# Performance work log

Hardware: AMD Instinct MI355X
Metric: run time of the kernel (lower is better)

## Reference

```python
import jax, jax.numpy as jnp
import numpy as np

B, N_VIS, N_TXT = 2, 2048, 256
N_HEAD, HEAD_DIM = 16, 64
C = N_HEAD * HEAD_DIM  # 1024
EPS = 1e-6


def setup_inputs() -> dict:
    key = jax.random.key(0)
    ks = jax.random.split(key, 24)
    s = 0.02
    inp = {
        'vis_x': jax.random.normal(ks[0], (B, N_VIS, C), jnp.float32),
        'txt_x': jax.random.normal(ks[1], (B, N_TXT, C), jnp.float32),
        'rope_cos': jax.random.uniform(ks[2], (N_VIS, HEAD_DIM), jnp.float32, -1.0, 1.0),
        'rope_sin': jax.random.uniform(ks[3], (N_VIS, HEAD_DIM), jnp.float32, -1.0, 1.0),
    }
    names = ['vis_qw', 'vis_kw', 'vis_vw', 'vis_ow', 'txt_qw', 'txt_kw', 'txt_vw', 'txt_ow']
    for i, n in enumerate(names):
        inp[n] = jax.random.normal(ks[4 + i], (C, C), jnp.float32) * s
        inp[n[:-1] + 'b'] = jnp.zeros((C,), jnp.float32)
    for n in ['vis_qn', 'vis_kn', 'txt_qn', 'txt_kn']:
        inp[n] = jnp.ones((HEAD_DIM,), jnp.float32)
    return inp


def _heads(x, w, b):
    # x: [B,N,C] -> [B,H,N,D]  (torch Linear: x @ W.T + b)
    y = x @ w.T + b
    Bn, N, _ = y.shape
    return y.reshape(Bn, N, N_HEAD, HEAD_DIM).transpose(0, 2, 1, 3)


def _rmsnorm(x, g):
    return x * jax.lax.rsqrt(jnp.mean(x * x, axis=-1, keepdims=True) + EPS) * g


def _rope(x, cos, sin):
    # interleaved-pair rotation: pairs (x0,x1) -> (-x1, x0)
    xr, xi = x[..., 0::2], x[..., 1::2]
    rot = jnp.stack([-xi, xr], axis=-1).reshape(x.shape)
    return x * cos[None, None] + rot * sin[None, None]


def reference(vis_x, txt_x, rope_cos, rope_sin,
              vis_qw, vis_qb, vis_kw, vis_kb, vis_vw, vis_vb, vis_ow, vis_ob,
              txt_qw, txt_qb, txt_kw, txt_kb, txt_vw, txt_vb, txt_ow, txt_ob,
              vis_qn, vis_kn, txt_qn, txt_kn):
    q_vis = _rmsnorm(_heads(vis_x, vis_qw, vis_qb), vis_qn)
    k_vis = _rmsnorm(_heads(vis_x, vis_kw, vis_kb), vis_kn)
    v_vis = _heads(vis_x, vis_vw, vis_vb)
    q_txt = _rmsnorm(_heads(txt_x, txt_qw, txt_qb), txt_qn)
    k_txt = _rmsnorm(_heads(txt_x, txt_kw, txt_kb), txt_kn)
    v_txt = _heads(txt_x, txt_vw, txt_vb)

    q_vis = _rope(q_vis, rope_cos, rope_sin)
    k_vis = _rope(k_vis, rope_cos, rope_sin)

    q = jnp.concatenate([q_txt, q_vis], axis=2)  # [B,H,S,D]
    k = jnp.concatenate([k_txt, k_vis], axis=2)
    v = jnp.concatenate([v_txt, v_vis], axis=2)

    scale = 1.0 / jnp.sqrt(jnp.asarray(HEAD_DIM, q.dtype))
    scores = jnp.einsum('bhqd,bhkd->bhqk', q, k) * scale
    attn = jax.nn.softmax(scores, axis=-1)
    out = jnp.einsum('bhqk,bhkd->bhqd', attn, v)  # [B,H,S,D]

    txt_out = out[:, :, :N_TXT, :].transpose(0, 2, 1, 3).reshape(q.shape[0], N_TXT, C)
    vis_out = out[:, :, N_TXT:, :].transpose(0, 2, 1, 3).reshape(q.shape[0], N_VIS, C)
    vis_out = vis_out @ vis_ow.T + vis_ob
    txt_out = txt_out @ txt_ow.T + txt_ob
    return (vis_out, txt_out)
```

## Files before the change

### kernel.cpp

```cpp
#include <hip/hip_runtime.h>

typedef _Float16 h8 __attribute__((ext_vector_type(8)));
typedef _Float16 h4 __attribute__((ext_vector_type(4)));
typedef _Float16 h2 __attribute__((ext_vector_type(2)));
typedef float f4 __attribute__((ext_vector_type(4)));
typedef float f16x16 __attribute__((ext_vector_type(16)));

#define LOG2E 1.44269504088896340736f

__device__ __forceinline__ void gload_lds16(const void* g, void* l) {
    __builtin_amdgcn_global_load_lds(
        (const __attribute__((address_space(1))) void*)g,
        (__attribute__((address_space(3))) void*)l, 16, 0, 0);
}

struct CastArgs { const float* src[10]; _Float16* dst[10]; };

__global__ __launch_bounds__(256) void cast_all_kernel(CastArgs a) {
    int blk = blockIdx.x;
    int seg, rel;
    if (blk < 4096)      { seg = 0; rel = blk; }
    else if (blk < 4608) { seg = 1; rel = blk - 4096; }
    else { int t = blk - 4608; seg = 2 + (t >> 10); rel = t & 1023; }
    long base = ((long)rel * 256 + threadIdx.x) * 4;
    float4 v = *(const float4*)(a.src[seg] + base);
    h4 o = { (_Float16)v.x, (_Float16)v.y, (_Float16)v.z, (_Float16)v.w };
    *(h4*)(a.dst[seg] + base) = o;
}

struct GemmDesc {
    const _Float16* A[2];
    const _Float16* W[2];
    char*           C[2];
    const float*    bias[2][3];
    long bsA[2];
    long aoff[2];
    long bsC[2];
    int  mshift[2];
    int  mcut;
};

template<bool OUT_F32>
__global__ __launch_bounds__(256)
void gemm_kernel(GemmDesc g, int K, int N)
{
    __shared__ __align__(16) _Float16 As[128 * 64];
    __shared__ __align__(16) _Float16 Bs[128 * 64];
    const int lane = threadIdx.x & 63;
    const int wave = threadIdx.x >> 6;
    const int mtile = blockIdx.y, ntile = blockIdx.x;

    const int seg = mtile >= g.mcut;
    const int mloc = mtile - (seg ? g.mcut : 0);
    const int bidx = mloc >> g.mshift[seg];
    const int min_ = mloc & ((1 << g.mshift[seg]) - 1);
    const _Float16* Ab = g.A[seg] + (long)bidx * g.bsA[seg] + g.aoff[seg]
                         + (long)min_ * 128 * K;
    const _Float16* Bb = g.W[seg] + (long)ntile * 128 * K;
    const long crow0 = (long)bidx * g.bsC[seg] + (long)min_ * 128 * N;

    const int wr = wave >> 1, wc = wave & 1;
    f4 acc[4][4] = {};

    for (int kt = 0; kt < K; kt += 64) {
        __syncthreads();
#pragma unroll
        for (int it = 0; it < 4; ++it) {
            int r = wave * 32 + it * 8 + (lane >> 3);
            int lc = (lane & 7) ^ (r & 7);
            gload_lds16((const char*)(Ab + (long)r * K + kt) + lc * 16,
                        (char*)As + (wave * 32 + it * 8) * 128);
            gload_lds16((const char*)(Bb + (long)r * K + kt) + lc * 16,
                        (char*)Bs + (wave * 32 + it * 8) * 128);
        }
        asm volatile("s_waitcnt vmcnt(0)" ::: "memory");
        __syncthreads();
#pragma unroll
        for (int kk = 0; kk < 2; ++kk) {
            h8 af[4], bf[4];
#pragma unroll
            for (int m = 0; m < 4; ++m) {
                int row = wr * 64 + m * 16 + (lane & 15);
                int pc = (kk * 4 + (lane >> 4)) ^ (row & 7);
                af[m] = *(const h8*)(&As[row * 64 + pc * 8]);
            }
#pragma unroll
            for (int n = 0; n < 4; ++n) {
                int row = wc * 64 + n * 16 + (lane & 15);
                int pc = (kk * 4 + (lane >> 4)) ^ (row & 7);
                bf[n] = *(const h8*)(&Bs[row * 64 + pc * 8]);
            }
#pragma unroll
            for (int m = 0; m < 4; ++m)
#pragma unroll
                for (int n = 0; n < 4; ++n)
                    acc[m][n] = __builtin_amdgcn_mfma_f32_16x16x32_f16(
                        af[m], bf[n], acc[m][n], 0, 0, 0);
        }
    }

#pragma unroll
    for (int n = 0; n < 4; ++n) {
        int col = ntile * 128 + wc * 64 + n * 16 + (lane & 15);
        const float* bp = (col < 1024) ? g.bias[seg][0]
                        : (col < 2048) ? g.bias[seg][1] : g.bias[seg][2];
        float bv = bp[col & 1023];
#pragma unroll
        for (int m = 0; m < 4; ++m) {
            int lrow = wr * 64 + m * 16 + ((lane >> 4) << 2);
#pragma unroll
            for (int r = 0; r < 4; ++r) {
                float v = acc[m][n][r] + bv;
                long off = crow0 + (long)(lrow + r) * N + col;
                if (OUT_F32) ((float*)g.C[seg])[off] = v;
                else         ((_Float16*)g.C[seg])[off] = (_Float16)v;
            }
        }
    }
}

__global__ __launch_bounds__(256)
void pass2_kernel(const _Float16* __restrict__ Yv, const _Float16* __restrict__ Yt,
                  const float* __restrict__ gqv, const float* __restrict__ gkv_,
                  const float* __restrict__ gqt, const float* __restrict__ gkt,
                  const float* __restrict__ rc, const float* __restrict__ rs,
                  _Float16* __restrict__ Q, _Float16* __restrict__ Kd,
                  _Float16* __restrict__ Vt)
{
    const int blk = blockIdx.x;
    const int is_vis = blk < 4096;
    const _Float16* Y; const float *gq, *gk; int m, nlog2;
    if (is_vis) { Y = Yv; gq = gqv; gk = gkv_; m = blk; nlog2 = 11; }
    else        { Y = Yt; gq = gqt; gk = gkt; m = blk - 4096; nlog2 = 8; }
    const int lane = threadIdx.x & 63;
    const int wave = threadIdx.x >> 6;
    const int b = m >> nlog2;
    const int n = m - (b << nlog2);
    const int npos = is_vis ? (256 + n) : n;
    const _Float16* y = Y + (long)m * 3072;
    const int d = lane;
    float cosv = 0.f, sinv = 0.f;
    if (is_vis) { cosv = rc[n * 64 + d]; sinv = rs[n * 64 + d]; }
    const float gqs = gq[d] * (0.125f * LOG2E);
    const float gks = gk[d];

#pragma unroll
    for (int hh = 0; hh < 4; ++hh) {
        int h = wave * 4 + hh;
        long ob = (((long)b * 16 + h) * 2304 + npos) * 64 + d;
        float q = (float)y[h * 64 + d];
        float ss = q * q;
#pragma unroll
        for (int o = 1; o < 64; o <<= 1) ss += __shfl_xor(ss, o);
        float qv = q * rsqrtf(ss * (1.0f / 64.0f) + 1e-6f) * gqs;
        if (is_vis) {
            float p = __shfl_xor(qv, 1);
            qv = qv * cosv + ((d & 1) ? p : -p) * sinv;
        }
        Q[ob] = (_Float16)qv;
        float k = (float)y[1024 + h * 64 + d];
        ss = k * k;
#pragma unroll
        for (int o = 1; o < 64; o <<= 1) ss += __shfl_xor(ss, o);
        float kv = k * rsqrtf(ss * (1.0f / 64.0f) + 1e-6f) * gks;
        if (is_vis) {
            float p = __shfl_xor(kv, 1);
            kv = kv * cosv + ((d & 1) ? p : -p) * sinv;
        }
        Kd[ob] = (_Float16)kv;
        float v = (float)y[2048 + h * 64 + d];
        Vt[(((long)b * 16 + h) * 64 + d) * 2304 + npos] = (_Float16)v;
    }
}

__device__ __forceinline__ void attn_stage(const char* Kt, const char* Vt, char* S,
                                           int bufB, int t,
                                           int gK0, int gK1, int gV0, int gV1,
                                           int ldsW) {
    const char* kt = Kt + (long)t * 8192;
    const char* vt = Vt + (long)t * 128;
    gload_lds16(kt + gK0, S + bufB + ldsW);
    gload_lds16(kt + gK1, S + bufB + 4096 + ldsW);
    gload_lds16(vt + gV0, S + 16384 + bufB + ldsW);
    gload_lds16(vt + gV1, S + 16384 + bufB + 4096 + ldsW);
}

__device__ __forceinline__ void attn_tile(const char* S, int bufB, const int* off,
                                          const h8* qf, f16x16* oacc, float& psum) {
    const f16x16 kZero = {};
    const h2 one2 = {(_Float16)1.f, (_Float16)1.f};
#pragma unroll
    for (int kblk = 0; kblk < 2; ++kblk) {
        f16x16 st;
        {
            h8 ka = *(const h8*)(S + bufB + kblk * 4096 + off[0]);
            st = __builtin_amdgcn_mfma_f32_32x32x16_f16(ka, qf[0], kZero, 0, 0, 0);
        }
#pragma unroll
        for (int ds = 1; ds < 4; ++ds) {
            h8 ka = *(const h8*)(S + bufB + kblk * 4096 + off[ds]);
            st = __builtin_amdgcn_mfma_f32_32x32x16_f16(ka, qf[ds], st, 0, 0, 0);
        }
        float p[16];
#pragma unroll
        for (int r = 0; r < 16; ++r) p[r] = exp2f(st[r]);
#pragma unroll
        for (int kb = 0; kb < 2; ++kb) {
            unsigned w0 = __builtin_bit_cast(unsigned,
                __builtin_amdgcn_cvt_pkrtz(p[8 * kb + 0], p[8 * kb + 1]));
            unsigned w1 = __builtin_bit_cast(unsigned,
                __builtin_amdgcn_cvt_pkrtz(p[8 * kb + 2], p[8 * kb + 3]));
            unsigned w2 = __builtin_bit_cast(unsigned,
                __builtin_amdgcn_cvt_pkrtz(p[8 * kb + 4], p[8 * kb + 5]));
            unsigned w3 = __builtin_bit_cast(unsigned,
                __builtin_amdgcn_cvt_pkrtz(p[8 * kb + 6], p[8 * kb + 7]));
            psum = __builtin_amdgcn_fdot2(__builtin_bit_cast(h2, w0), one2, psum, false);
            psum = __builtin_amdgcn_fdot2(__builtin_bit_cast(h2, w1), one2, psum, false);
            psum = __builtin_amdgcn_fdot2(__builtin_bit_cast(h2, w2), one2, psum, false);
            psum = __builtin_amdgcn_fdot2(__builtin_bit_cast(h2, w3), one2, psum, false);
            asm("v_permlane32_swap_b32 %0, %1" : "+v"(w0), "+v"(w2));
            asm("v_permlane32_swap_b32 %0, %1" : "+v"(w1), "+v"(w3));
            union { unsigned u[4]; h8 v; } pa;
            pa.u[0] = w0; pa.u[1] = w1; pa.u[2] = w2; pa.u[3] = w3;
#pragma unroll
            for (int dblk = 0; dblk < 2; ++dblk) {
                h8 vb = *(const h8*)(S + 16384 + bufB + dblk * 4096 + off[kblk * 2 + kb]);
                oacc[dblk] = __builtin_amdgcn_mfma_f32_32x32x16_f16(
                    pa.v, vb, oacc[dblk], 0, 0, 0);
            }
        }
    }
}

__global__ __launch_bounds__(256)
void attn_kernel(const _Float16* __restrict__ Qg,
                 const _Float16* __restrict__ Kg,
                 const _Float16* __restrict__ Vg,
                 _Float16* __restrict__ Op,
                 float* __restrict__ Lp)
{
    __shared__ __align__(16) char S[32768];
    const int lane = threadIdx.x & 63;
    const int wave = threadIdx.x >> 6;
    const int l31 = lane & 31, hi = lane >> 5;
    const int d0 = blockIdx.x;
    const int id = (d0 & 7) * 144 + (d0 >> 3);
    const int split = id / 576;
    const int rem = id - split * 576;
    const int bh = rem / 18;
    const int qb = rem - bh * 18;
    const int b = bh >> 4, h = bh & 15;
    const _Float16* Qbh = Qg + (long)bh * 2304 * 64;
    const char* Kt = (const char*)(Kg + (long)bh * 2304 * 64) + (long)split * 1152 * 128;
    const char* Vt = (const char*)(Vg + (long)bh * 64 * 2304) + (long)split * 1152 * 2;
    _Float16* Ops = Op + (long)split * 4718592;
    float* Lps = Lp + (long)split * 73728;
    const int q0 = qb * 128 + wave * 32;

    h8 qf[4];
#pragma unroll
    for (int ds = 0; ds < 4; ++ds)
        qf[ds] = *(const h8*)(Qbh + (long)(q0 + l31) * 64 + ds * 16 + hi * 8);

    const int sg16 = ((lane & 7) ^ (lane >> 3)) * 16;
    const int rK = wave * 8 + (lane >> 3);
    const int gK0 = rK * 128 + sg16;
    const int gK1 = gK0 + 32 * 128;
    const int gV0 = rK * 4608 + sg16;
    const int gV1 = gV0 + 32 * 4608;
    const int ldsW = wave * 1024;
    int off[4];
#pragma unroll
    for (int j = 0; j < 4; ++j)
        off[j] = l31 * 128 + (((j * 2 + hi) ^ (l31 & 7)) * 16);

    f16x16 oacc[2] = {};
    float psum = 0.f;

    attn_stage(Kt, Vt, S, 0, 0, gK0, gK1, gV0, gV1, ldsW);
    asm volatile("s_waitcnt vmcnt(0)" ::: "memory");
    __syncthreads();

#pragma unroll 1
    for (int pr = 0; pr < 9; ++pr) {
        const int t = pr * 2;
        attn_stage(Kt, Vt, S, 8192, t + 1, gK0, gK1, gV0, gV1, ldsW);
        __builtin_amdgcn_s_setprio(1);
        attn_tile(S, 0, off, qf, oacc, psum);
        __builtin_amdgcn_s_setprio(0);
        asm volatile("s_waitcnt vmcnt(0)" ::: "memory");
        __syncthreads();
        if (pr != 8)
            attn_stage(Kt, Vt, S, 0, t + 2, gK0, gK1, gV0, gV1, ldsW);
        __builtin_amdgcn_s_setprio(1);
        attn_tile(S, 8192, off, qf, oacc, psum);
        __builtin_amdgcn_s_setprio(0);
        asm volatile("s_waitcnt vmcnt(0)" ::: "memory");
        __syncthreads();
    }

    float lsum = psum + __shfl_xor(psum, 32);
    if (hi == 0) Lps[(long)bh * 2304 + q0 + l31] = lsum;
#pragma unroll
    for (int dblk = 0; dblk < 2; ++dblk) {
        int dcol = h * 64 + dblk * 32 + l31;
#pragma unroll
        for (int r = 0; r < 16; ++r) {
            int qrow = q0 + (r & 3) + 8 * (r >> 2) + 4 * hi;
            Ops[((long)b * 2304 + qrow) * 1024 + dcol] = (_Float16)oacc[dblk][r];
        }
    }
}

__global__ __launch_bounds__(256)
void combine_kernel(const _Float16* __restrict__ Op,
                    const float* __restrict__ Lp,
                    _Float16* __restrict__ Oh)
{
    long i = ((long)blockIdx.x * 256 + threadIdx.x) * 8;
    h8 a = *(const h8*)(Op + i);
    h8 c = *(const h8*)(Op + 4718592 + i);
    long row = i >> 10;
    int bb = row >= 2304;
    int n = (int)row - bb * 2304;
    int h = ((int)i & 1023) >> 6;
    long lidx = ((long)(bb * 16 + h)) * 2304 + n;
    float inv = 1.0f / (Lp[lidx] + Lp[73728 + lidx]);
    h8 o;
#pragma unroll
    for (int j = 0; j < 8; ++j)
        o[j] = (_Float16)(((float)a[j] + (float)c[j]) * inv);
    *(h8*)(Oh + i) = o;
}

extern "C" void kernel_launch(void* const* d_in, const int* in_sizes, int n_in,
                              void* d_out, int out_size, void* d_ws, size_t ws_size,
                              hipStream_t stream)
{
    const float* vis_x    = (const float*)d_in[0];
    const float* txt_x    = (const float*)d_in[1];
    const float* rope_cos = (const float*)d_in[2];
    const float* rope_sin = (const float*)d_in[3];
    const float* vis_qw = (const float*)d_in[4];
    const float* vis_qb = (const float*)d_in[5];
    const float* vis_kw = (const float*)d_in[6];
    const float* vis_kb = (const float*)d_in[7];
    const float* vis_vw = (const float*)d_in[8];
    const float* vis_vb = (const float*)d_in[9];
    const float* vis_ow = (const float*)d_in[10];
    const float* vis_ob = (const float*)d_in[11];
    const float* txt_qw = (const float*)d_in[12];
    const float* txt_qb = (const float*)d_in[13];
    const float* txt_kw = (const float*)d_in[14];
    const float* txt_kb = (const float*)d_in[15];
    const float* txt_vw = (const float*)d_in[16];
    const float* txt_vb = (const float*)d_in[17];
    const float* txt_ow = (const float*)d_in[18];
    const float* txt_ob = (const float*)d_in[19];
    const float* vis_qn = (const float*)d_in[20];
    const float* vis_kn = (const float*)d_in[21];
    const float* txt_qn = (const float*)d_in[22];
    const float* txt_kn = (const float*)d_in[23];

    char* ws = (char*)d_ws;
    _Float16* Xvis  = (_Float16*)(ws);
    _Float16* Xtxt  = (_Float16*)(ws + 8388608);
    _Float16* Qh    = (_Float16*)(ws);
    _Float16* WqkvV = (_Float16*)(ws + 9437184);
    _Float16* WqkvT = (_Float16*)(ws + 15728640);
    _Float16* WoV   = (_Float16*)(ws + 22020096);
    _Float16* WoT   = (_Float16*)(ws + 24117248);
    _Float16* Yvis  = (_Float16*)(ws + 26214400);
    _Float16* Ytxt  = (_Float16*)(ws + 51380224);
    _Float16* OpP   = (_Float16*)(ws + 26214400);
    float*    LpP   = (float*)   (ws + 45088768);
    _Float16* Oh    = (_Float16*)(ws + 26214400);
    _Float16* Kh    = (_Float16*)(ws + 54525952);
    _Float16* Vth   = (_Float16*)(ws + 63963136);

    CastArgs ca;
    ca.src[0] = vis_x;  ca.dst[0] = Xvis;
    ca.src[1] = txt_x;  ca.dst[1] = Xtxt;
    ca.src[2] = vis_qw; ca.dst[2] = WqkvV;
    ca.src[3] = vis_kw; ca.dst[3] = WqkvV + 1048576;
    ca.src[4] = vis_vw; ca.dst[4] = WqkvV + 2097152;
    ca.src[5] = txt_qw; ca.dst[5] = WqkvT;
    ca.src[6] = txt_kw; ca.dst[6] = WqkvT + 1048576;
    ca.src[7] = txt_vw; ca.dst[7] = WqkvT + 2097152;
    ca.src[8] = vis_ow; ca.dst[8] = WoV;
    ca.src[9] = txt_ow; ca.dst[9] = WoT;
    cast_all_kernel<<<12800, 256, 0, stream>>>(ca);

    GemmDesc gq;
    gq.A[0] = Xvis;  gq.A[1] = Xtxt;
    gq.W[0] = WqkvV; gq.W[1] = WqkvT;
    gq.C[0] = (char*)Yvis; gq.C[1] = (char*)Ytxt;
    gq.bias[0][0] = vis_qb; gq.bias[0][1] = vis_kb; gq.bias[0][2] = vis_vb;
    gq.bias[1][0] = txt_qb; gq.bias[1][1] = txt_kb; gq.bias[1][2] = txt_vb;
    gq.bsA[0] = 0; gq.bsA[1] = 0;
    gq.aoff[0] = 0; gq.aoff[1] = 0;
    gq.bsC[0] = 0; gq.bsC[1] = 0;
    gq.mshift[0] = 5; gq.mshift[1] = 5;
    gq.mcut = 32;
    gemm_kernel<false><<<dim3(24, 36), 256, 0, stream>>>(gq, 1024, 3072);

    pass2_kernel<<<4608, 256, 0, stream>>>(
        Yvis, Ytxt, vis_qn, vis_kn, txt_qn, txt_kn, rope_cos, rope_sin,
        Qh, Kh, Vth);

    attn_kernel<<<1152, 256, 0, stream>>>(Qh, Kh, Vth, OpP, LpP);
    combine_kernel<<<2304, 256, 0, stream>>>(OpP, LpP, Oh);

    GemmDesc go;
    go.A[0] = Oh; go.A[1] = Oh;
    go.W[0] = WoV; go.W[1] = WoT;
    go.C[0] = (char*)d_out; go.C[1] = (char*)((float*)d_out + 4194304);
    go.bias[0][0] = vis_ob; go.bias[0][1] = vis_ob; go.bias[0][2] = vis_ob;
    go.bias[1][0] = txt_ob; go.bias[1][1] = txt_ob; go.bias[1][2] = txt_ob;
    go.bsA[0] = 2359296;  go.bsA[1] = 2359296;
    go.aoff[0] = 262144;  go.aoff[1] = 0;
    go.bsC[0] = 2097152;  go.bsC[1] = 262144;
    go.mshift[0] = 4; go.mshift[1] = 1;
    go.mcut = 32;
    gemm_kernel<true><<<dim3(8, 36), 256, 0, stream>>>(go, 1024, 1024);
}
```

Baseline: 199.6 us.

## Remap GEMM tiles per XCD, vectorize norm/rope pass, widen attention split-K

The GEMM grid becomes 1D and is remapped so each XCD works on a contiguous block of M/N tiles, aiming at better L2 reuse. The norm/RoPE pass now handles one row per wave with 8-wide vector loads and stores instead of per-element shuffles. Attention can split the KV range four ways instead of two when the workspace is large enough, issues the two score MFMA chains interleaved, and sets a launch-bounds occupancy hint. The combine kernel is generalized to sum a variable number of splits, at the cost of extra partial-output traffic.

```diff
diff --git a/kernel.cpp b/kernel.cpp
--- a/kernel.cpp
+++ b/kernel.cpp
@@ -42,13 +42,17 @@
 
 template<bool OUT_F32>
 __global__ __launch_bounds__(256)
-void gemm_kernel(GemmDesc g, int K, int N)
+void gemm_kernel(GemmDesc g, int K, int N, int gm, int gn, int xgn)
 {
     __shared__ __align__(16) _Float16 As[128 * 64];
     __shared__ __align__(16) _Float16 Bs[128 * 64];
     const int lane = threadIdx.x & 63;
     const int wave = threadIdx.x >> 6;
-    const int mtile = blockIdx.y, ntile = blockIdx.x;
+    const int lid = blockIdx.x;
+    const int xcd = lid & 7;
+    const int r0 = lid >> 3;
+    const int mtile = (xcd / xgn) * gm + (r0 % gm);
+    const int ntile = (xcd % xgn) * gn + (r0 / gm);
 
     const int seg = mtile >= g.mcut;
     const int mloc = mtile - (seg ? g.mcut : 0);
@@ -119,6 +123,36 @@
     }
 }
 
+__device__ __forceinline__ float ssum8(h8 v) {
+    float s = 0.f;
+#pragma unroll
+    for (int j = 0; j < 8; ++j) { float f = (float)v[j]; s += f * f; }
+    return s;
+}
+__device__ __forceinline__ float red8(float s) {
+    s += __shfl_xor(s, 1); s += __shfl_xor(s, 2); s += __shfl_xor(s, 4);
+    return s;
+}
+__device__ __forceinline__ h8 norm_rope(h8 v, float rs_, const float* g, float gmul,
+                                        const float* cs, const float* sn, int vis) {
+    float f[8];
+#pragma unroll
+    for (int j = 0; j < 8; ++j) f[j] = (float)v[j] * rs_ * g[j] * gmul;
+    h8 o;
+    if (vis) {
+#pragma unroll
+        for (int j = 0; j < 8; j += 2) {
+            float a = f[j], b = f[j + 1];
+            o[j]     = (_Float16)(a * cs[j]     - b * sn[j]);
+            o[j + 1] = (_Float16)(b * cs[j + 1] + a * sn[j + 1]);
+        }
+    } else {
+#pragma unroll
+        for (int j = 0; j < 8; ++j) o[j] = (_Float16)f[j];
+    }
+    return o;
+}
+
 __global__ __launch_bounds__(256)
 void pass2_kernel(const _Float16* __restrict__ Yv, const _Float16* __restrict__ Yt,
                   const float* __restrict__ gqv, const float* __restrict__ gkv_,
@@ -127,49 +161,63 @@
                   _Float16* __restrict__ Q, _Float16* __restrict__ Kd,
                   _Float16* __restrict__ Vt)
 {
-    const int blk = blockIdx.x;
-    const int is_vis = blk < 4096;
-    const _Float16* Y; const float *gq, *gk; int m, nlog2;
-    if (is_vis) { Y = Yv; gq = gqv; gk = gkv_; m = blk; nlog2 = 11; }
-    else        { Y = Yt; gq = gqt; gk = gkt; m = blk - 4096; nlog2 = 8; }
+    const int wave = threadIdx.x >> 6;
     const int lane = threadIdx.x & 63;
-    const int wave = threadIdx.x >> 6;
-    const int b = m >> nlog2;
-    const int n = m - (b << nlog2);
-    const int npos = is_vis ? (256 + n) : n;
-    const _Float16* y = Y + (long)m * 3072;
-    const int d = lane;
-    float cosv = 0.f, sinv = 0.f;
-    if (is_vis) { cosv = rc[n * 64 + d]; sinv = rs[n * 64 + d]; }
-    const float gqs = gq[d] * (0.125f * LOG2E);
-    const float gks = gk[d];
-
-#pragma unroll
-    for (int hh = 0; hh < 4; ++hh) {
-        int h = wave * 4 + hh;
-        long ob = (((long)b * 16 + h) * 2304 + npos) * 64 + d;
-        float q = (float)y[h * 64 + d];
-        float ss = q * q;
-#pragma unroll
-        for (int o = 1; o < 64; o <<= 1) ss += __shfl_xor(ss, o);
-        float qv = q * rsqrtf(ss * (1.0f / 64.0f) + 1e-6f) * gqs;
-        if (is_vis) {
-            float p = __shfl_xor(qv, 1);
-            qv = qv * cosv + ((d & 1) ? p : -p) * sinv;
-        }
-        Q[ob] = (_Float16)qv;
-        float k = (float)y[1024 + h * 64 + d];
-        ss = k * k;
-#pragma unroll
-        for (int o = 1; o < 64; o <<= 1) ss += __shfl_xor(ss, o);
-        float kv = k * rsqrtf(ss * (1.0f / 64.0f) + 1e-6f) * gks;
-        if (is_vis) {
-            float p = __shfl_xor(kv, 1);
-            kv = kv * cosv + ((d & 1) ? p : -p) * sinv;
-        }
-        Kd[ob] = (_Float16)kv;
-        float v = (float)y[2048 + h * 64 + d];
-        Vt[(((long)b * 16 + h) * 64 + d) * 2304 + npos] = (_Float16)v;
+    const int row = blockIdx.x * 4 + wave;
+    const int is_vis = row < 4096;
+    const _Float16* y;
+    const float *gq, *gk;
+    int b, n, npos;
+    if (is_vis) {
+        y = Yv + (long)row * 3072; gq = gqv; gk = gkv_;
+        b = row >> 11; n = row & 2047; npos = 256 + n;
+    } else {
+        int r2 = row - 4096;
+        y = Yt + (long)r2 * 3072; gq = gqt; gk = gkt;
+        b = r2 >> 8; n = r2 & 255; npos = n;
+    }
+    const int h0 = lane >> 3;
+    const int d0 = (lane & 7) * 8;
+
+    h8 q0 = *(const h8*)(y + lane * 8);
+    h8 q1 = *(const h8*)(y + 512 + lane * 8);
+    h8 k0 = *(const h8*)(y + 1024 + lane * 8);
+    h8 k1 = *(const h8*)(y + 1536 + lane * 8);
+    h8 v0 = *(const h8*)(y + 2048 + lane * 8);
+    h8 v1 = *(const h8*)(y + 2560 + lane * 8);
+
+    float ga[8], gb[8];
+    *(float4*)(ga)     = *(const float4*)(gq + d0);
+    *(float4*)(ga + 4) = *(const float4*)(gq + d0 + 4);
+    *(float4*)(gb)     = *(const float4*)(gk + d0);
+    *(float4*)(gb + 4) = *(const float4*)(gk + d0 + 4);
+    float cs[8], sn[8];
+    if (is_vis) {
+        *(float4*)(cs)     = *(const float4*)(rc + n * 64 + d0);
+        *(float4*)(cs + 4) = *(const float4*)(rc + n * 64 + d0 + 4);
+        *(float4*)(sn)     = *(const float4*)(rs + n * 64 + d0);
+        *(float4*)(sn + 4) = *(const float4*)(rs + n * 64 + d0 + 4);
+    }
+
+    const float rq0 = rsqrtf(red8(ssum8(q0)) * (1.0f / 64.0f) + 1e-6f);
+    const float rq1 = rsqrtf(red8(ssum8(q1)) * (1.0f / 64.0f) + 1e-6f);
+    const float rk0 = rsqrtf(red8(ssum8(k0)) * (1.0f / 64.0f) + 1e-6f);
+    const float rk1 = rsqrtf(red8(ssum8(k1)) * (1.0f / 64.0f) + 1e-6f);
+
+    const float qmul = 0.125f * LOG2E;
+    const long obA = (((long)b * 16 + h0)      * 2304 + npos) * 64 + d0;
+    const long obB = (((long)b * 16 + h0 + 8)  * 2304 + npos) * 64 + d0;
+    *(h8*)(Q + obA)  = norm_rope(q0, rq0, ga, qmul, cs, sn, is_vis);
+    *(h8*)(Q + obB)  = norm_rope(q1, rq1, ga, qmul, cs, sn, is_vis);
+    *(h8*)(Kd + obA) = norm_rope(k0, rk0, gb, 1.0f, cs, sn, is_vis);
+    *(h8*)(Kd + obB) = norm_rope(k1, rk1, gb, 1.0f, cs, sn, is_vis);
+
+    const long vbA = ((long)(b * 16 + h0)     * 64 + d0) * 2304 + npos;
+    const long vbB = ((long)(b * 16 + h0 + 8) * 64 + d0) * 2304 + npos;
+#pragma unroll
+    for (int j = 0; j < 8; ++j) {
+        Vt[vbA + (long)j * 2304] = v0[j];
+        Vt[vbB + (long)j * 2304] = v1[j];
     }
 }
 
@@ -185,74 +233,83 @@
     gload_lds16(vt + gV1, S + 16384 + bufB + 4096 + ldsW);
 }
 
+__device__ __forceinline__ void pv_half(const float* p, const char* S, int vbase,
+                                        const int* off, int kblk,
+                                        f16x16* oacc, float& psum) {
+    const h2 one2 = {(_Float16)1.f, (_Float16)1.f};
+#pragma unroll
+    for (int kb = 0; kb < 2; ++kb) {
+        unsigned w0 = __builtin_bit_cast(unsigned,
+            __builtin_amdgcn_cvt_pkrtz(p[8 * kb + 0], p[8 * kb + 1]));
+        unsigned w1 = __builtin_bit_cast(unsigned,
+            __builtin_amdgcn_cvt_pkrtz(p[8 * kb + 2], p[8 * kb + 3]));
+        unsigned w2 = __builtin_bit_cast(unsigned,
+            __builtin_amdgcn_cvt_pkrtz(p[8 * kb + 4], p[8 * kb + 5]));
+        unsigned w3 = __builtin_bit_cast(unsigned,
+            __builtin_amdgcn_cvt_pkrtz(p[8 * kb + 6], p[8 * kb + 7]));
+        psum = __builtin_amdgcn_fdot2(__builtin_bit_cast(h2, w0), one2, psum, false);
+        psum = __builtin_amdgcn_fdot2(__builtin_bit_cast(h2, w1), one2, psum, false);
+        psum = __builtin_amdgcn_fdot2(__builtin_bit_cast(h2, w2), one2, psum, false);
+        psum = __builtin_amdgcn_fdot2(__builtin_bit_cast(h2, w3), one2, psum, false);
+        asm("v_permlane32_swap_b32 %0, %1" : "+v"(w0), "+v"(w2));
+        asm("v_permlane32_swap_b32 %0, %1" : "+v"(w1), "+v"(w3));
+        union { unsigned u[4]; h8 v; } pa;
+        pa.u[0] = w0; pa.u[1] = w1; pa.u[2] = w2; pa.u[3] = w3;
+#pragma unroll
+        for (int dblk = 0; dblk < 2; ++dblk) {
+            h8 vb = *(const h8*)(S + vbase + dblk * 4096 + off[kblk * 2 + kb]);
+            oacc[dblk] = __builtin_amdgcn_mfma_f32_32x32x16_f16(
+                pa.v, vb, oacc[dblk], 0, 0, 0);
+        }
+    }
+}
+
 __device__ __forceinline__ void attn_tile(const char* S, int bufB, const int* off,
                                           const h8* qf, f16x16* oacc, float& psum) {
     const f16x16 kZero = {};
-    const h2 one2 = {(_Float16)1.f, (_Float16)1.f};
-#pragma unroll
-    for (int kblk = 0; kblk < 2; ++kblk) {
-        f16x16 st;
-        {
-            h8 ka = *(const h8*)(S + bufB + kblk * 4096 + off[0]);
-            st = __builtin_amdgcn_mfma_f32_32x32x16_f16(ka, qf[0], kZero, 0, 0, 0);
-        }
-#pragma unroll
-        for (int ds = 1; ds < 4; ++ds) {
-            h8 ka = *(const h8*)(S + bufB + kblk * 4096 + off[ds]);
-            st = __builtin_amdgcn_mfma_f32_32x32x16_f16(ka, qf[ds], st, 0, 0, 0);
-        }
-        float p[16];
-#pragma unroll
-        for (int r = 0; r < 16; ++r) p[r] = exp2f(st[r]);
-#pragma unroll
-        for (int kb = 0; kb < 2; ++kb) {
-            unsigned w0 = __builtin_bit_cast(unsigned,
-                __builtin_amdgcn_cvt_pkrtz(p[8 * kb + 0], p[8 * kb + 1]));
-            unsigned w1 = __builtin_bit_cast(unsigned,
-                __builtin_amdgcn_cvt_pkrtz(p[8 * kb + 2], p[8 * kb + 3]));
-            unsigned w2 = __builtin_bit_cast(unsigned,
-                __builtin_amdgcn_cvt_pkrtz(p[8 * kb + 4], p[8 * kb + 5]));
-            unsigned w3 = __builtin_bit_cast(unsigned,
-                __builtin_amdgcn_cvt_pkrtz(p[8 * kb + 6], p[8 * kb + 7]));
-            psum = __builtin_amdgcn_fdot2(__builtin_bit_cast(h2, w0), one2, psum, false);
-            psum = __builtin_amdgcn_fdot2(__builtin_bit_cast(h2, w1), one2, psum, false);
-            psum = __builtin_amdgcn_fdot2(__builtin_bit_cast(h2, w2), one2, psum, false);
-            psum = __builtin_amdgcn_fdot2(__builtin_bit_cast(h2, w3), one2, psum, false);
-            asm("v_permlane32_swap_b32 %0, %1" : "+v"(w0), "+v"(w2));
-            asm("v_permlane32_swap_b32 %0, %1" : "+v"(w1), "+v"(w3));
-            union { unsigned u[4]; h8 v; } pa;
-            pa.u[0] = w0; pa.u[1] = w1; pa.u[2] = w2; pa.u[3] = w3;
-#pragma unroll
-            for (int dblk = 0; dblk < 2; ++dblk) {
-                h8 vb = *(const h8*)(S + 16384 + bufB + dblk * 4096 + off[kblk * 2 + kb]);
-                oacc[dblk] = __builtin_amdgcn_mfma_f32_32x32x16_f16(
-                    pa.v, vb, oacc[dblk], 0, 0, 0);
-            }
-        }
-    }
-}
-
-__global__ __launch_bounds__(256)
+    f16x16 st0, st1;
+    {
+        h8 ka0 = *(const h8*)(S + bufB + off[0]);
+        h8 ka1 = *(const h8*)(S + bufB + 4096 + off[0]);
+        st0 = __builtin_amdgcn_mfma_f32_32x32x16_f16(ka0, qf[0], kZero, 0, 0, 0);
+        st1 = __builtin_amdgcn_mfma_f32_32x32x16_f16(ka1, qf[0], kZero, 0, 0, 0);
+    }
+#pragma unroll
+    for (int ds = 1; ds < 4; ++ds) {
+        h8 ka0 = *(const h8*)(S + bufB + off[ds]);
+        h8 ka1 = *(const h8*)(S + bufB + 4096 + off[ds]);
+        st0 = __builtin_amdgcn_mfma_f32_32x32x16_f16(ka0, qf[ds], st0, 0, 0, 0);
+        st1 = __builtin_amdgcn_mfma_f32_32x32x16_f16(ka1, qf[ds], st1, 0, 0, 0);
+    }
+    float p0[16], p1[16];
+#pragma unroll
+    for (int r = 0; r < 16; ++r) { p0[r] = exp2f(st0[r]); p1[r] = exp2f(st1[r]); }
+    pv_half(p0, S, 16384 + bufB, off, 0, oacc, psum);
+    pv_half(p1, S, 16384 + bufB, off, 1, oacc, psum);
+}
+
+__global__ __launch_bounds__(256, 4)
 void attn_kernel(const _Float16* __restrict__ Qg,
                  const _Float16* __restrict__ Kg,
                  const _Float16* __restrict__ Vg,
                  _Float16* __restrict__ Op,
-                 float* __restrict__ Lp)
+                 float* __restrict__ Lp,
+                 int nt, int cpx)
 {
     __shared__ __align__(16) char S[32768];
     const int lane = threadIdx.x & 63;
     const int wave = threadIdx.x >> 6;
     const int l31 = lane & 31, hi = lane >> 5;
     const int d0 = blockIdx.x;
-    const int id = (d0 & 7) * 144 + (d0 >> 3);
+    const int id = (d0 & 7) * cpx + (d0 >> 3);
     const int split = id / 576;
     const int rem = id - split * 576;
     const int bh = rem / 18;
     const int qb = rem - bh * 18;
     const int b = bh >> 4, h = bh & 15;
     const _Float16* Qbh = Qg + (long)bh * 2304 * 64;
-    const char* Kt = (const char*)(Kg + (long)bh * 2304 * 64) + (long)split * 1152 * 128;
-    const char* Vt = (const char*)(Vg + (long)bh * 64 * 2304) + (long)split * 1152 * 2;
+    const char* Kt = (const char*)(Kg + (long)bh * 2304 * 64) + (long)split * nt * 8192;
+    const char* Vt = (const char*)(Vg + (long)bh * 64 * 2304) + (long)split * nt * 128;
     _Float16* Ops = Op + (long)split * 4718592;
     float* Lps = Lp + (long)split * 73728;
     const int q0 = qb * 128 + wave * 32;
@@ -281,22 +338,37 @@
     asm volatile("s_waitcnt vmcnt(0)" ::: "memory");
     __syncthreads();
 
+    int t = 0;
 #pragma unroll 1
-    for (int pr = 0; pr < 9; ++pr) {
-        const int t = pr * 2;
+    for (int pr = 0; pr < (nt - 1) >> 1; ++pr) {
         attn_stage(Kt, Vt, S, 8192, t + 1, gK0, gK1, gV0, gV1, ldsW);
         __builtin_amdgcn_s_setprio(1);
         attn_tile(S, 0, off, qf, oacc, psum);
         __builtin_amdgcn_s_setprio(0);
         asm volatile("s_waitcnt vmcnt(0)" ::: "memory");
         __syncthreads();
-        if (pr != 8)
-            attn_stage(Kt, Vt, S, 0, t + 2, gK0, gK1, gV0, gV1, ldsW);
+        attn_stage(Kt, Vt, S, 0, t + 2, gK0, gK1, gV0, gV1, ldsW);
         __builtin_amdgcn_s_setprio(1);
         attn_tile(S, 8192, off, qf, oacc, psum);
         __builtin_amdgcn_s_setprio(0);
         asm volatile("s_waitcnt vmcnt(0)" ::: "memory");
         __syncthreads();
+        t += 2;
+    }
+    if (nt & 1) {
+        __builtin_amdgcn_s_setprio(1);
+        attn_tile(S, 0, off, qf, oacc, psum);
+        __builtin_amdgcn_s_setprio(0);
+    } else {
+        attn_stage(Kt, Vt, S, 8192, nt - 1, gK0, gK1, gV0, gV1, ldsW);
+        __builtin_amdgcn_s_setprio(1);
+        attn_tile(S, 0, off, qf, oacc, psum);
+        __builtin_amdgcn_s_setprio(0);
+        asm volatile("s_waitcnt vmcnt(0)" ::: "memory");
+        __syncthreads();
+        __builtin_amdgcn_s_setprio(1);
+        attn_tile(S, 8192, off, qf, oacc, psum);
+        __builtin_amdgcn_s_setprio(0);
     }
 
     float lsum = psum + __shfl_xor(psum, 32);
@@ -315,21 +387,26 @@
 __global__ __launch_bounds__(256)
 void combine_kernel(const _Float16* __restrict__ Op,
                     const float* __restrict__ Lp,
-                    _Float16* __restrict__ Oh)
+                    _Float16* __restrict__ Oh, int ns)
 {
     long i = ((long)blockIdx.x * 256 + threadIdx.x) * 8;
-    h8 a = *(const h8*)(Op + i);
-    h8 c = *(const h8*)(Op + 4718592 + i);
     long row = i >> 10;
     int bb = row >= 2304;
     int n = (int)row - bb * 2304;
     int h = ((int)i & 1023) >> 6;
     long lidx = ((long)(bb * 16 + h)) * 2304 + n;
-    float inv = 1.0f / (Lp[lidx] + Lp[73728 + lidx]);
+    float l = 0.f;
+    float acc[8] = {};
+    for (int s = 0; s < ns; ++s) {
+        l += Lp[(long)s * 73728 + lidx];
+        h8 a = *(const h8*)(Op + (long)s * 4718592 + i);
+#pragma unroll
+        for (int j = 0; j < 8; ++j) acc[j] += (float)a[j];
+    }
+    float inv = 1.0f / l;
     h8 o;
 #pragma unroll
-    for (int j = 0; j < 8; ++j)
-        o[j] = (_Float16)(((float)a[j] + (float)c[j]) * inv);
+    for (int j = 0; j < 8; ++j) o[j] = (_Float16)(acc[j] * inv);
     *(h8*)(Oh + i) = o;
 }
 
@@ -372,11 +449,16 @@
     _Float16* WoT   = (_Float16*)(ws + 24117248);
     _Float16* Yvis  = (_Float16*)(ws + 26214400);
     _Float16* Ytxt  = (_Float16*)(ws + 51380224);
-    _Float16* OpP   = (_Float16*)(ws + 26214400);
-    float*    LpP   = (float*)   (ws + 45088768);
-    _Float16* Oh    = (_Float16*)(ws + 26214400);
     _Float16* Kh    = (_Float16*)(ws + 54525952);
     _Float16* Vth   = (_Float16*)(ws + 63963136);
+
+    const int ns = (ws_size >= 112328704) ? 4 : 2;
+    const int nt = (ns == 4) ? 9 : 18;
+    _Float16* OpP;
+    if (ns == 4) OpP = (_Float16*)(ws + 73400320);
+    else         OpP = (_Float16*)(ws + 26214400);
+    float* LpP = (float*)((char*)OpP + (size_t)ns * 9437184);
+    _Float16* Oh = OpP;
 
     CastArgs ca;
     ca.src[0] = vis_x;  ca.dst[0] = Xvis;
@@ -402,14 +484,14 @@
     gq.bsC[0] = 0; gq.bsC[1] = 0;
     gq.mshift[0] = 5; gq.mshift[1] = 5;
     gq.mcut = 32;
-    gemm_kernel<false><<<dim3(24, 36), 256, 0, stream>>>(gq, 1024, 3072);
-
-    pass2_kernel<<<4608, 256, 0, stream>>>(
+    gemm_kernel<false><<<864, 256, 0, stream>>>(gq, 1024, 3072, 9, 12, 2);
+
+    pass2_kernel<<<1152, 256, 0, stream>>>(
         Yvis, Ytxt, vis_qn, vis_kn, txt_qn, txt_kn, rope_cos, rope_sin,
         Qh, Kh, Vth);
 
-    attn_kernel<<<1152, 256, 0, stream>>>(Qh, Kh, Vth, OpP, LpP);
-    combine_kernel<<<2304, 256, 0, stream>>>(OpP, LpP, Oh);
+    attn_kernel<<<576 * ns, 256, 0, stream>>>(Qh, Kh, Vth, OpP, LpP, nt, 72 * ns);
+    combine_kernel<<<2304, 256, 0, stream>>>(OpP, LpP, Oh, ns);
 
     GemmDesc go;
     go.A[0] = Oh; go.A[1] = Oh;
@@ -422,5 +504,5 @@
     go.bsC[0] = 2097152;  go.bsC[1] = 262144;
     go.mshift[0] = 4; go.mshift[1] = 1;
     go.mcut = 32;
-    gemm_kernel<true><<<dim3(8, 36), 256, 0, stream>>>(go, 1024, 1024);
-}
+    gemm_kernel<true><<<288, 256, 0, stream>>>(go, 1024, 1024, 9, 4, 2);
+}
```

Result: no change. 196.0 us (-1.8%).
